# Performance work log

Measured on AMD Instinct MI355X. Metric: run time of the kernel, lower is better.

The kernel has to match this reference:

```python
import jax, jax.numpy as jnp
import numpy as np

RBF_GAMMA = 0.001  # initial_gamma_value
DIAG_VALUE = 0.1


def setup_inputs() -> dict:
    key = jax.random.key(0)
    k_x, k_w1, k_b1, k_w2 = jax.random.split(key, 4)
    B, N, T, D = 8, 4096, 128, 32  # batch, nodes, in_dim, latent_dim
    x = jax.random.normal(k_x, (B, N, T), dtype=jnp.float32)
    # nn.Linear params; stored as (in, out) so proj = x @ W + b
    W1 = jax.random.normal(k_w1, (T, D), dtype=jnp.float32) * (2.0 / T) ** 0.5
    W2 = jax.random.normal(k_w2, (T, D), dtype=jnp.float32) * (2.0 / T) ** 0.5
    b1 = jnp.zeros((D,), dtype=jnp.float32)
    b2 = jnp.zeros((D,), dtype=jnp.float32)
    return {"x": x, "W1": W1, "b1": b1, "W2": W2, "b2": b2}


def reference(x, W1, b1, W2, b2):
    # proj1, proj2: (B, N, D)
    p1 = jnp.einsum("bnt,td->bnd", x, W1) + b1
    p2 = jnp.einsum("bnt,td->bnd", x, W2) + b2
    # RBF kernel: exp(-gamma * ||p1_i - p2_j||^2), computed via the
    # algebraic rewrite ||a||^2 + ||b||^2 - 2 a.b (no (B,N,N,D) diff tensor).
    sq1 = jnp.sum(p1 * p1, axis=-1)  # (B, N)
    sq2 = jnp.sum(p2 * p2, axis=-1)  # (B, N)
    dot = jnp.einsum("bnd,bmd->bnm", p1, p2)  # (B, N, N)
    dist_sq = jnp.maximum(sq1[:, :, None] + sq2[:, None, :] - 2.0 * dot, 0.0)
    sim = jnp.exp(-RBF_GAMMA * dist_sq)  # (B, N, N)
    sim = sim.mean(axis=0)  # (N, N)
    # fill_diagonal_(0.1)
    n = sim.shape[0]
    idx = jnp.arange(n)
    sim = sim.at[idx, idx].set(DIAG_VALUE)
    return sim
```

## Files before the change

### kernel.cpp

```cpp
#include <hip/hip_runtime.h>
#include <hip/hip_bf16.h>

typedef __bf16 bf16x8 __attribute__((ext_vector_type(8)));
typedef float  f32x4  __attribute__((ext_vector_type(4)));

constexpr int B = 8, N = 4096, T = 128, D = 32;
constexpr float GAMMA = 0.001f;
constexpr float LOG2E = 1.4426950408889634f;
constexpr float K2 = -GAMMA * LOG2E;
constexpr float M2 = -2.0f * K2;

__device__ __forceinline__ float exp2_fast(float t) {
#if __has_builtin(__builtin_amdgcn_exp2f)
  return __builtin_amdgcn_exp2f(t);
#else
  return exp2f(t);
#endif
}

__device__ __forceinline__ float exp2_poly(float t) {
  return fmaf(fmaf(fmaf(0.0285860f, t, 0.2107500f), t, 0.6821055f), t,
              0.9993455f);
}

__global__ __launch_bounds__(256, 2) void proj_mfma(
    const float* __restrict__ x,  const float* __restrict__ W1,
    const float* __restrict__ b1, const float* __restrict__ W2,
    const float* __restrict__ b2,
    __bf16* __restrict__ p1b, __bf16* __restrict__ p2b,
    float* __restrict__ s1, float* __restrict__ e2) {
  __shared__ bf16x8 wlds[4][4][64];
  const int tid  = threadIdx.x;
  const int lane = tid & 63;
  const int wid  = tid >> 6;
  const int lr   = lane & 15;
  const int lk   = lane >> 4;
  const int r0   = blockIdx.x * 64 + wid * 16;

  #pragma unroll
  for (int t = 0; t < 4; ++t) {
    const int e  = tid + t * 256;
    const int c  = e >> 8;
    const int s  = (e >> 6) & 3;
    const int ln = e & 63;
    const int llr = ln & 15, llk = ln >> 4;
    const float* Wp = (c < 2) ? W1 : W2;
    const int cc = (c * 16 + llr) & 31;
    bf16x8 v;
    #pragma unroll
    for (int j = 0; j < 8; ++j)
      v[j] = (__bf16)Wp[(s * 32 + llk * 8 + j) * D + cc];
    wlds[c][s][ln] = v;
  }
  __syncthreads();

  bf16x8 wf[4][4];
  #pragma unroll
  for (int c = 0; c < 4; ++c)
    #pragma unroll
    for (int s = 0; s < 4; ++s)
      wf[c][s] = wlds[c][s][lane];

  bf16x8 af[4];
  const float* xr = x + (size_t)(r0 + lr) * T;
  #pragma unroll
  for (int s = 0; s < 4; ++s) {
    const int t0 = s * 32 + lk * 8;
    const f32x4 v0 = *reinterpret_cast<const f32x4*>(xr + t0);
    const f32x4 v1 = *reinterpret_cast<const f32x4*>(xr + t0 + 4);
    #pragma unroll
    for (int j = 0; j < 4; ++j) {
      af[s][j]     = (__bf16)v0[j];
      af[s][4 + j] = (__bf16)v1[j];
    }
  }

  f32x4 pv[4];
  #pragma unroll
  for (int c = 0; c < 4; ++c) {
    const float* bp = (c < 2) ? b1 : b2;
    const float bv = bp[(c * 16 + lr) & 31];
    f32x4 accv = {bv, bv, bv, bv};
    #pragma unroll
    for (int s = 0; s < 4; ++s)
      accv = __builtin_amdgcn_mfma_f32_16x16x32_bf16(af[s], wf[c][s], accv, 0, 0, 0);
    pv[c] = accv;
  }

  #pragma unroll
  for (int c = 0; c < 2; ++c)
    #pragma unroll
    for (int r = 0; r < 4; ++r)
      p1b[(size_t)(r0 + lk * 4 + r) * D + c * 16 + lr] = (__bf16)(M2 * pv[c][r]);
  #pragma unroll
  for (int c = 2; c < 4; ++c)
    #pragma unroll
    for (int r = 0; r < 4; ++r)
      p2b[(size_t)(r0 + lk * 4 + r) * D + (c - 2) * 16 + lr] = (__bf16)pv[c][r];

  float q1[4], q2[4];
  #pragma unroll
  for (int r = 0; r < 4; ++r) {
    q1[r] = fmaf(pv[0][r], pv[0][r], pv[1][r] * pv[1][r]);
    q2[r] = fmaf(pv[2][r], pv[2][r], pv[3][r] * pv[3][r]);
  }
  #pragma unroll
  for (int m = 1; m < 16; m <<= 1)
    #pragma unroll
    for (int r = 0; r < 4; ++r) {
      q1[r] += __shfl_xor(q1[r], m, 64);
      q2[r] += __shfl_xor(q2[r], m, 64);
    }
  if (lr == 0) {
    #pragma unroll
    for (int r = 0; r < 4; ++r) {
      const int row = r0 + lk * 4 + r;
      s1[row] = K2 * q1[r];
      e2[row] = 0.125f * exp2_fast(K2 * q2[r]);
    }
  }
}

__global__ __launch_bounds__(256, 4) void fused_kernel(
    const __bf16* __restrict__ p1b, const __bf16* __restrict__ p2b,
    const float* __restrict__ s1,   const float* __restrict__ e2,
    float* __restrict__ out) {
  const int lane = threadIdx.x & 63;
  const int wid  = threadIdx.x >> 6;
  const int j0 = blockIdx.x * 64;
  const int i0 = blockIdx.y * 128 + wid * 32;
  const int lr = lane & 15;
  const int lk = lane >> 4;

  const __bf16* pa = p1b + (size_t)(i0 + lr) * D + lk * 8;
  const __bf16* pb = p2b + (size_t)(j0 + lr) * D + lk * 8;
  const float*  ps = s1 + i0 + lk * 4;
  const float*  pe = e2 + j0 + lr;

  f32x4 acc[2][4];
  #pragma unroll
  for (int a = 0; a < 2; ++a)
    #pragma unroll
    for (int c = 0; c < 4; ++c)
      acc[a][c] = f32x4{0.f, 0.f, 0.f, 0.f};

  #pragma unroll
  for (int b = 0; b < B; ++b) {
    const size_t ob = (size_t)b * (N * D);
    const size_t os = (size_t)b * N;

    bf16x8 A[2];
    #pragma unroll
    for (int a = 0; a < 2; ++a)
      A[a] = *reinterpret_cast<const bf16x8*>(pa + ob + a * (16 * D));
    bf16x8 Bf[4];
    #pragma unroll
    for (int c = 0; c < 4; ++c)
      Bf[c] = *reinterpret_cast<const bf16x8*>(pb + ob + c * (16 * D));
    f32x4 S[2];
    #pragma unroll
    for (int a = 0; a < 2; ++a)
      S[a] = *reinterpret_cast<const f32x4*>(ps + os + a * 16);
    float E[4];
    #pragma unroll
    for (int c = 0; c < 4; ++c)
      E[c] = pe[os + c * 16];

    #pragma unroll
    for (int a = 0; a < 2; ++a) {
      #pragma unroll
      for (int c = 0; c < 4; ++c) {
        f32x4 t = __builtin_amdgcn_mfma_f32_16x16x32_bf16(
            A[a], Bf[c], S[a], 0, 0, 0);
        #pragma unroll
        for (int r = 0; r < 4; ++r)
          acc[a][c][r] = fmaf(E[c], exp2_poly(t[r]), acc[a][c][r]);
      }
    }
  }

  const bool hasdiag = (i0 < j0 + 64) && (j0 < i0 + 32);
  #pragma unroll
  for (int a = 0; a < 2; ++a) {
    #pragma unroll
    for (int c = 0; c < 4; ++c) {
      #pragma unroll
      for (int r = 0; r < 4; ++r) {
        const int row = i0 + a * 16 + lk * 4 + r;
        const int col = j0 + c * 16 + lr;
        float v = acc[a][c][r];
        if (hasdiag && row == col) v = 0.1f;
        out[(size_t)row * N + col] = v;
      }
    }
  }
}

extern "C" void kernel_launch(void* const* d_in, const int* in_sizes, int n_in,
                              void* d_out, int out_size, void* d_ws, size_t ws_size,
                              hipStream_t stream) {
  (void)in_sizes; (void)n_in; (void)out_size; (void)ws_size;
  const float* x  = (const float*)d_in[0];
  const float* W1 = (const float*)d_in[1];
  const float* b1 = (const float*)d_in[2];
  const float* W2 = (const float*)d_in[3];
  const float* b2 = (const float*)d_in[4];
  float* out = (float*)d_out;

  char* ws = (char*)d_ws;
  const size_t pbytes = (size_t)B * N * D * sizeof(__bf16);
  __bf16* p1b = (__bf16*)ws;
  __bf16* p2b = (__bf16*)(ws + pbytes);
  float*  s1  = (float*)(ws + 2 * pbytes);
  float*  e2  = (float*)(ws + 2 * pbytes + (size_t)B * N * sizeof(float));

  proj_mfma<<<(B * N) / 64, 256, 0, stream>>>(x, W1, b1, W2, b2, p1b, p2b, s1, e2);

  dim3 grid(N / 64, N / 128);
  fused_kernel<<<grid, 256, 0, stream>>>(p1b, p2b, s1, e2, out);
}
```

Measured before the change: 46.52 us.

## Stage shared B-operand tiles in LDS and preload all A fragments

The fused kernel now cooperatively loads the block's p2 tiles for all batches into LDS with an XOR swizzle, along with the s1 and e2 vectors. Each wave then preloads its p1 fragments for all eight batches into registers before the compute loop. This replaces repeated per-wave global loads of the same B, S and E data with a single shared copy and moves all global latency before the loop. The cost is about 40 KB of LDS per block, more registers, and a lower occupancy hint (3 blocks instead of 4).

Measured after the change: 37.33 us. 19.7% less time.

```diff
diff --git a/kernel.cpp b/kernel.cpp
--- a/kernel.cpp
+++ b/kernel.cpp
@@ -121,21 +121,54 @@
   }
 }
 
-__global__ __launch_bounds__(256, 4) void fused_kernel(
+__global__ __launch_bounds__(256, 3) void fused_kernel(
     const __bf16* __restrict__ p1b, const __bf16* __restrict__ p2b,
     const float* __restrict__ s1,   const float* __restrict__ e2,
     float* __restrict__ out) {
-  const int lane = threadIdx.x & 63;
-  const int wid  = threadIdx.x >> 6;
+  __shared__ __align__(16) __bf16 LB[B * 64 * 32];
+  __shared__ __align__(16) float  LS[B * 128];
+  __shared__ __align__(16) float  LE[B * 64];
+
+  const int tid  = threadIdx.x;
+  const int lane = tid & 63;
+  const int wid  = tid >> 6;
   const int j0 = blockIdx.x * 64;
-  const int i0 = blockIdx.y * 128 + wid * 32;
+  const int i0blk = blockIdx.y * 128;
+  const int i0 = i0blk + wid * 32;
   const int lr = lane & 15;
   const int lk = lane >> 4;
 
-  const __bf16* pa = p1b + (size_t)(i0 + lr) * D + lk * 8;
-  const __bf16* pb = p2b + (size_t)(j0 + lr) * D + lk * 8;
-  const float*  ps = s1 + i0 + lk * 4;
-  const float*  pe = e2 + j0 + lr;
+  #pragma unroll
+  for (int q = 0; q < 8; ++q) {
+    const int g   = tid + q * 256;
+    const int b   = g >> 8;
+    const int c8  = g & 255;
+    const int row = c8 >> 2;
+    const int sl  = c8 & 3;
+    const bf16x8 v = *reinterpret_cast<const bf16x8*>(
+        p2b + ((size_t)b * N + j0 + row) * D + sl * 8);
+    const int su = sl ^ ((row >> 1) & 3);
+    *reinterpret_cast<bf16x8*>(&LB[(((b << 6) + row) << 2 | su) << 3]) = v;
+  }
+  {
+    const int b = tid >> 5, o = (tid & 31) * 4;
+    *reinterpret_cast<f32x4*>(&LS[b * 128 + o]) =
+        *reinterpret_cast<const f32x4*>(s1 + (size_t)b * N + i0blk + o);
+  }
+  if (tid < 128) {
+    const int b = tid >> 4, o = (tid & 15) * 4;
+    *reinterpret_cast<f32x4*>(&LE[b * 64 + o]) =
+        *reinterpret_cast<const f32x4*>(e2 + (size_t)b * N + j0 + o);
+  }
+  bf16x8 Areg[B][2];
+  #pragma unroll
+  for (int b = 0; b < B; ++b)
+    #pragma unroll
+    for (int a = 0; a < 2; ++a)
+      Areg[b][a] = *reinterpret_cast<const bf16x8*>(
+          p1b + ((size_t)b * N + i0 + a * 16 + lr) * D + lk * 8);
+
+  __syncthreads();
 
   f32x4 acc[2][4];
   #pragma unroll
@@ -144,34 +177,30 @@
     for (int c = 0; c < 4; ++c)
       acc[a][c] = f32x4{0.f, 0.f, 0.f, 0.f};
 
+  const int sub = lk ^ ((lr >> 1) & 3);
   #pragma unroll
   for (int b = 0; b < B; ++b) {
-    const size_t ob = (size_t)b * (N * D);
-    const size_t os = (size_t)b * N;
-
-    bf16x8 A[2];
+    bf16x8 Bf[4];
+    #pragma unroll
+    for (int c = 0; c < 4; ++c)
+      Bf[c] = *reinterpret_cast<const bf16x8*>(
+          &LB[(((b << 6) + c * 16 + lr) << 2 | sub) << 3]);
+    f32x4 S[2];
     #pragma unroll
     for (int a = 0; a < 2; ++a)
-      A[a] = *reinterpret_cast<const bf16x8*>(pa + ob + a * (16 * D));
-    bf16x8 Bf[4];
+      S[a] = *reinterpret_cast<const f32x4*>(
+          &LS[b * 128 + wid * 32 + a * 16 + lk * 4]);
+    float E[4];
     #pragma unroll
     for (int c = 0; c < 4; ++c)
-      Bf[c] = *reinterpret_cast<const bf16x8*>(pb + ob + c * (16 * D));
-    f32x4 S[2];
-    #pragma unroll
-    for (int a = 0; a < 2; ++a)
-      S[a] = *reinterpret_cast<const f32x4*>(ps + os + a * 16);
-    float E[4];
-    #pragma unroll
-    for (int c = 0; c < 4; ++c)
-      E[c] = pe[os + c * 16];
+      E[c] = LE[b * 64 + c * 16 + lr];
 
     #pragma unroll
     for (int a = 0; a < 2; ++a) {
       #pragma unroll
       for (int c = 0; c < 4; ++c) {
         f32x4 t = __builtin_amdgcn_mfma_f32_16x16x32_bf16(
-            A[a], Bf[c], S[a], 0, 0, 0);
+            Areg[b][a], Bf[c], S[a], 0, 0, 0);
         #pragma unroll
         for (int r = 0; r < 4; ++r)
           acc[a][c][r] = fmaf(E[c], exp2_poly(t[r]), acc[a][c][r]);
```

## Restructure RBF kernel into single-wave blocks with register-resident A and double-buffered B loads

Applied to the files above, without the earlier changes.

The fused similarity kernel becomes one 64-thread wave per block. Each wave holds its 32-row p1 fragments and s1 values for all batches in registers and sweeps 128 columns in 16-column steps. The p2/e2 fragments for the next step are loaded while the current step computes, so global-load latency overlaps the MFMA and exp work. This raises register use (A and S for 8 batches plus two fragment buffers) and makes each store narrower, in exchange for loading the A side once per block.

Result: slower. 73.18 us (+57.3%).

```diff
diff --git a/kernel.cpp b/kernel.cpp
--- a/kernel.cpp
+++ b/kernel.cpp
@@ -121,79 +121,93 @@
   }
 }
 
-__global__ __launch_bounds__(256, 4) void fused_kernel(
+struct Frag {
+  bf16x8 Bv[B];
+  float  Ev[B];
+};
+
+__global__ __launch_bounds__(64, 2) void fused_kernel(
     const __bf16* __restrict__ p1b, const __bf16* __restrict__ p2b,
     const float* __restrict__ s1,   const float* __restrict__ e2,
     float* __restrict__ out) {
-  const int lane = threadIdx.x & 63;
-  const int wid  = threadIdx.x >> 6;
-  const int j0 = blockIdx.x * 64;
-  const int i0 = blockIdx.y * 128 + wid * 32;
+  const int lane = threadIdx.x;
+  const int bid  = blockIdx.x;
+  const int is   = bid & 127;
+  const int jc   = bid >> 7;
+  const int i0   = is * 32;
+  const int jb   = jc * 128;
   const int lr = lane & 15;
   const int lk = lane >> 4;
 
-  const __bf16* pa = p1b + (size_t)(i0 + lr) * D + lk * 8;
-  const __bf16* pb = p2b + (size_t)(j0 + lr) * D + lk * 8;
-  const float*  ps = s1 + i0 + lk * 4;
-  const float*  pe = e2 + j0 + lr;
-
-  f32x4 acc[2][4];
-  #pragma unroll
-  for (int a = 0; a < 2; ++a)
-    #pragma unroll
-    for (int c = 0; c < 4; ++c)
-      acc[a][c] = f32x4{0.f, 0.f, 0.f, 0.f};
-
+  bf16x8 A[B][2];
+  f32x4  S[B][2];
   #pragma unroll
   for (int b = 0; b < B; ++b) {
-    const size_t ob = (size_t)b * (N * D);
-    const size_t os = (size_t)b * N;
-
-    bf16x8 A[2];
-    #pragma unroll
-    for (int a = 0; a < 2; ++a)
-      A[a] = *reinterpret_cast<const bf16x8*>(pa + ob + a * (16 * D));
-    bf16x8 Bf[4];
-    #pragma unroll
-    for (int c = 0; c < 4; ++c)
-      Bf[c] = *reinterpret_cast<const bf16x8*>(pb + ob + c * (16 * D));
-    f32x4 S[2];
-    #pragma unroll
-    for (int a = 0; a < 2; ++a)
-      S[a] = *reinterpret_cast<const f32x4*>(ps + os + a * 16);
-    float E[4];
-    #pragma unroll
-    for (int c = 0; c < 4; ++c)
-      E[c] = pe[os + c * 16];
-
     #pragma unroll
     for (int a = 0; a < 2; ++a) {
+      A[b][a] = *reinterpret_cast<const bf16x8*>(
+          p1b + ((size_t)b * N + i0 + a * 16 + lr) * D + lk * 8);
+      S[b][a] = *reinterpret_cast<const f32x4*>(
+          s1 + (size_t)b * N + i0 + a * 16 + lk * 4);
+    }
+  }
+
+  Frag fx, fy;
+
+  auto load = [&](Frag& f, int st) __attribute__((always_inline)) {
+    const int jj = jb + st * 16;
+    #pragma unroll
+    for (int b = 0; b < B; ++b) {
+      f.Bv[b] = *reinterpret_cast<const bf16x8*>(
+          p2b + ((size_t)b * N + jj + lr) * D + lk * 8);
+      f.Ev[b] = e2[(size_t)b * N + jj + lr];
+    }
+  };
+
+  auto computeStore = [&](const Frag& f, int st) __attribute__((always_inline)) {
+    const int jj = jb + st * 16;
+    f32x4 acc0 = {0.f, 0.f, 0.f, 0.f};
+    f32x4 acc1 = {0.f, 0.f, 0.f, 0.f};
+    #pragma unroll
+    for (int b = 0; b < B; ++b) {
+      f32x4 t0 = __builtin_amdgcn_mfma_f32_16x16x32_bf16(
+          A[b][0], f.Bv[b], S[b][0], 0, 0, 0);
       #pragma unroll
-      for (int c = 0; c < 4; ++c) {
-        f32x4 t = __builtin_amdgcn_mfma_f32_16x16x32_bf16(
-            A[a], Bf[c], S[a], 0, 0, 0);
-        #pragma unroll
-        for (int r = 0; r < 4; ++r)
-          acc[a][c][r] = fmaf(E[c], exp2_poly(t[r]), acc[a][c][r]);
-      }
-    }
-  }
-
-  const bool hasdiag = (i0 < j0 + 64) && (j0 < i0 + 32);
-  #pragma unroll
-  for (int a = 0; a < 2; ++a) {
-    #pragma unroll
-    for (int c = 0; c < 4; ++c) {
+      for (int r = 0; r < 4; ++r)
+        acc0[r] = fmaf(f.Ev[b], exp2_poly(t0[r]), acc0[r]);
+      f32x4 t1 = __builtin_amdgcn_mfma_f32_16x16x32_bf16(
+          A[b][1], f.Bv[b], S[b][1], 0, 0, 0);
       #pragma unroll
-      for (int r = 0; r < 4; ++r) {
-        const int row = i0 + a * 16 + lk * 4 + r;
-        const int col = j0 + c * 16 + lr;
-        float v = acc[a][c][r];
-        if (hasdiag && row == col) v = 0.1f;
-        out[(size_t)row * N + col] = v;
-      }
-    }
-  }
+      for (int r = 0; r < 4; ++r)
+        acc1[r] = fmaf(f.Ev[b], exp2_poly(t1[r]), acc1[r]);
+    }
+    const bool hasdiag = (jj < i0 + 32) && (i0 < jj + 16);
+    const int col = jj + lr;
+    #pragma unroll
+    for (int r = 0; r < 4; ++r) {
+      const int row0 = i0 + lk * 4 + r;
+      float v0 = acc0[r];
+      if (hasdiag && row0 == col) v0 = 0.1f;
+      out[(size_t)row0 * N + col] = v0;
+    }
+    #pragma unroll
+    for (int r = 0; r < 4; ++r) {
+      const int row1 = i0 + 16 + lk * 4 + r;
+      float v1 = acc1[r];
+      if (hasdiag && row1 == col) v1 = 0.1f;
+      out[(size_t)row1 * N + col] = v1;
+    }
+  };
+
+  load(fx, 0);
+  load(fy, 1); computeStore(fx, 0);
+  load(fx, 2); computeStore(fy, 1);
+  load(fy, 3); computeStore(fx, 2);
+  load(fx, 4); computeStore(fy, 3);
+  load(fy, 5); computeStore(fx, 4);
+  load(fx, 6); computeStore(fy, 5);
+  load(fy, 7); computeStore(fx, 6);
+  computeStore(fy, 7);
 }
 
 extern "C" void kernel_launch(void* const* d_in, const int* in_sizes, int n_in,
@@ -216,6 +230,5 @@
 
   proj_mfma<<<(B * N) / 64, 256, 0, stream>>>(x, W1, b1, W2, b2, p1b, p2b, s1, e2);
 
-  dim3 grid(N / 64, N / 128);
-  fused_kernel<<<grid, 256, 0, stream>>>(p1b, p2b, s1, e2, out);
-}
+  fused_kernel<<<(N / 32) * (N / 128), 64, 0, stream>>>(p1b, p2b, s1, e2, out);
+}
```

## Shrink fused kernel to single-wave 16x64 tiles with batched 4-batch loads

Applied to the files above, without the earlier changes.

The fused kernel now runs one wavefront per block, with each block covering a 16x64 output tile instead of four waves covering 128x64. Blocks are indexed through a 1D grid that walks row strips fastest. The batch loop is split into two passes of four, and each pass issues all of its loads before any MFMA/exp work, to raise memory-level parallelism. In exchange, each wave reuses less data (one A fragment per batch), launches many more small blocks, and holds more registers for the prefetched fragments.

Result: slower. 63.37 us (+36.2%).

```diff
diff --git a/kernel.cpp b/kernel.cpp
--- a/kernel.cpp
+++ b/kernel.cpp
@@ -121,77 +121,70 @@
   }
 }
 
-__global__ __launch_bounds__(256, 4) void fused_kernel(
+__global__ __launch_bounds__(64, 2) void fused_kernel(
     const __bf16* __restrict__ p1b, const __bf16* __restrict__ p2b,
     const float* __restrict__ s1,   const float* __restrict__ e2,
     float* __restrict__ out) {
-  const int lane = threadIdx.x & 63;
-  const int wid  = threadIdx.x >> 6;
-  const int j0 = blockIdx.x * 64;
-  const int i0 = blockIdx.y * 128 + wid * 32;
+  const int lane = threadIdx.x;
+  const int bid  = blockIdx.x;
+  const int is   = bid & 255;
+  const int jc   = bid >> 8;
+  const int i0   = is * 16;
+  const int j0   = jc * 64;
   const int lr = lane & 15;
   const int lk = lane >> 4;
 
-  const __bf16* pa = p1b + (size_t)(i0 + lr) * D + lk * 8;
-  const __bf16* pb = p2b + (size_t)(j0 + lr) * D + lk * 8;
-  const float*  ps = s1 + i0 + lk * 4;
-  const float*  pe = e2 + j0 + lr;
-
-  f32x4 acc[2][4];
-  #pragma unroll
-  for (int a = 0; a < 2; ++a)
-    #pragma unroll
-    for (int c = 0; c < 4; ++c)
-      acc[a][c] = f32x4{0.f, 0.f, 0.f, 0.f};
-
-  #pragma unroll
-  for (int b = 0; b < B; ++b) {
-    const size_t ob = (size_t)b * (N * D);
-    const size_t os = (size_t)b * N;
-
-    bf16x8 A[2];
-    #pragma unroll
-    for (int a = 0; a < 2; ++a)
-      A[a] = *reinterpret_cast<const bf16x8*>(pa + ob + a * (16 * D));
-    bf16x8 Bf[4];
-    #pragma unroll
-    for (int c = 0; c < 4; ++c)
-      Bf[c] = *reinterpret_cast<const bf16x8*>(pb + ob + c * (16 * D));
-    f32x4 S[2];
-    #pragma unroll
-    for (int a = 0; a < 2; ++a)
-      S[a] = *reinterpret_cast<const f32x4*>(ps + os + a * 16);
-    float E[4];
-    #pragma unroll
-    for (int c = 0; c < 4; ++c)
-      E[c] = pe[os + c * 16];
-
-    #pragma unroll
-    for (int a = 0; a < 2; ++a) {
-      #pragma unroll
-      for (int c = 0; c < 4; ++c) {
-        f32x4 t = __builtin_amdgcn_mfma_f32_16x16x32_bf16(
-            A[a], Bf[c], S[a], 0, 0, 0);
-        #pragma unroll
-        for (int r = 0; r < 4; ++r)
-          acc[a][c][r] = fmaf(E[c], exp2_poly(t[r]), acc[a][c][r]);
-      }
-    }
-  }
-
-  const bool hasdiag = (i0 < j0 + 64) && (j0 < i0 + 32);
-  #pragma unroll
-  for (int a = 0; a < 2; ++a) {
-    #pragma unroll
-    for (int c = 0; c < 4; ++c) {
-      #pragma unroll
-      for (int r = 0; r < 4; ++r) {
-        const int row = i0 + a * 16 + lk * 4 + r;
-        const int col = j0 + c * 16 + lr;
-        float v = acc[a][c][r];
-        if (hasdiag && row == col) v = 0.1f;
-        out[(size_t)row * N + col] = v;
-      }
+  f32x4 acc[4];
+  #pragma unroll
+  for (int c = 0; c < 4; ++c) acc[c] = f32x4{0.f, 0.f, 0.f, 0.f};
+
+#define PASS(B0)                                                              \
+  {                                                                           \
+    bf16x8 A[4];                                                              \
+    bf16x8 Bf[4][4];                                                          \
+    f32x4  S[4];                                                              \
+    float  E[4][4];                                                           \
+    _Pragma("unroll")                                                         \
+    for (int b4 = 0; b4 < 4; ++b4) {                                          \
+      const size_t rb = (size_t)(B0 + b4) * N;                                \
+      A[b4] = *reinterpret_cast<const bf16x8*>(                               \
+          p1b + (rb + i0 + lr) * D + lk * 8);                                 \
+      _Pragma("unroll")                                                       \
+      for (int c = 0; c < 4; ++c)                                             \
+        Bf[b4][c] = *reinterpret_cast<const bf16x8*>(                         \
+            p2b + (rb + j0 + c * 16 + lr) * D + lk * 8);                      \
+      S[b4] = *reinterpret_cast<const f32x4*>(s1 + rb + i0 + lk * 4);         \
+      _Pragma("unroll")                                                       \
+      for (int c = 0; c < 4; ++c)                                             \
+        E[b4][c] = e2[rb + j0 + c * 16 + lr];                                 \
+    }                                                                         \
+    _Pragma("unroll")                                                         \
+    for (int b4 = 0; b4 < 4; ++b4) {                                          \
+      _Pragma("unroll")                                                       \
+      for (int c = 0; c < 4; ++c) {                                           \
+        f32x4 t = __builtin_amdgcn_mfma_f32_16x16x32_bf16(                    \
+            A[b4], Bf[b4][c], S[b4], 0, 0, 0);                                \
+        _Pragma("unroll")                                                     \
+        for (int r = 0; r < 4; ++r)                                           \
+          acc[c][r] = fmaf(E[b4][c], exp2_poly(t[r]), acc[c][r]);             \
+      }                                                                       \
+    }                                                                         \
+  }
+
+  PASS(0)
+  PASS(4)
+#undef PASS
+
+  const bool hasdiag = (i0 < j0 + 64) && (j0 < i0 + 16);
+  #pragma unroll
+  for (int c = 0; c < 4; ++c) {
+    #pragma unroll
+    for (int r = 0; r < 4; ++r) {
+      const int row = i0 + lk * 4 + r;
+      const int col = j0 + c * 16 + lr;
+      float v = acc[c][r];
+      if (hasdiag && row == col) v = 0.1f;
+      out[(size_t)row * N + col] = v;
     }
   }
 }
@@ -216,6 +209,5 @@
 
   proj_mfma<<<(B * N) / 64, 256, 0, stream>>>(x, W1, b1, W2, b2, p1b, p2b, s1, e2);
 
-  dim3 grid(N / 64, N / 128);
-  fused_kernel<<<grid, 256, 0, stream>>>(p1b, p2b, s1, e2, out);
-}
+  fused_kernel<<<(N / 16) * (N / 64), 64, 0, stream>>>(p1b, p2b, s1, e2, out);
+}
```
